# Kernel optimization log

Measured on AMD Instinct MI355X. Metric: run time of the kernel, lower is better.

## Reference

```python
import jax, jax.numpy as jnp
import numpy as np

# static config (matches init_kwargs and spatial_shapes input)
SPATIAL = ((100, 100), (50, 50), (25, 25), (13, 13))  # (H, W) per level
D_MODEL, N_HEADS, N_LEVELS, N_POINTS, D_FFN = 256, 8, 4, 4, 1024
D_HEAD = D_MODEL // N_HEADS
LEN_IN = sum(h * w for h, w in SPATIAL)
LEVEL_START = np.cumsum([0] + [h * w for h, w in SPATIAL])[:-1]


def setup_inputs() -> dict:
    key = jax.random.key(0)
    ks = jax.random.split(key, 12)
    N = 2
    f = lambda k, shape, s=0.02: jax.random.normal(k, shape, jnp.float32) * s
    return {
        "src": jax.random.normal(ks[0], (N, LEN_IN, D_MODEL), jnp.float32),
        "pos": jax.random.normal(ks[1], (N, LEN_IN, D_MODEL), jnp.float32),
        "reference_points": jax.random.uniform(ks[2], (N, LEN_IN, N_LEVELS, 2), jnp.float32),
        "spatial_shapes": jnp.asarray(SPATIAL, jnp.int32),
        "level_start_index": jnp.asarray(LEVEL_START, jnp.int32),
        "W_value": f(ks[3], (D_MODEL, D_MODEL)),
        "b_value": jnp.zeros((D_MODEL,), jnp.float32),
        "W_off": f(ks[4], (D_MODEL, N_HEADS * N_LEVELS * N_POINTS * 2)),
        "b_off": f(ks[5], (N_HEADS * N_LEVELS * N_POINTS * 2,), 0.5),
        "W_attn": f(ks[6], (D_MODEL, N_HEADS * N_LEVELS * N_POINTS)),
        "b_attn": jnp.zeros((N_HEADS * N_LEVELS * N_POINTS,), jnp.float32),
        "W_out": f(ks[7], (D_MODEL, D_MODEL)),
        "b_out": jnp.zeros((D_MODEL,), jnp.float32),
        "W1": f(ks[8], (D_MODEL, D_FFN)),
        "b1": jnp.zeros((D_FFN,), jnp.float32),
        "W2": f(ks[9], (D_FFN, D_MODEL)),
        "b2": jnp.zeros((D_MODEL,), jnp.float32),
        "g1": jnp.ones((D_MODEL,), jnp.float32),
        "be1": jnp.zeros((D_MODEL,), jnp.float32),
        "g2": jnp.ones((D_MODEL,), jnp.float32),
        "be2": jnp.zeros((D_MODEL,), jnp.float32),
    }


def _ln(x, g, b, eps=1e-5):
    mu = x.mean(-1, keepdims=True)
    var = ((x - mu) ** 2).mean(-1, keepdims=True)
    return (x - mu) * jax.lax.rsqrt(var + eps) * g + b


def _bilinear(v, loc, H, W):
    # v: [N, heads, H*W, Dh]; loc: [N, Lq, heads, P, 2] normalized to [0,1]
    # replicates F.grid_sample(align_corners=False, padding_mode='zeros') with grid=2*loc-1
    N, Lq, Hh, P, _ = loc.shape
    x = loc[..., 0] * W - 0.5
    y = loc[..., 1] * H - 0.5
    x0 = jnp.floor(x)
    y0 = jnp.floor(y)
    wx1 = x - x0
    wy1 = y - y0
    x0i = x0.astype(jnp.int32)
    y0i = y0.astype(jnp.int32)
    out = jnp.zeros((N, Lq, Hh, P, v.shape[-1]), v.dtype)
    for dy, dx in ((0, 0), (0, 1), (1, 0), (1, 1)):
        xi = x0i + dx
        yi = y0i + dy
        w = (wx1 if dx else 1.0 - wx1) * (wy1 if dy else 1.0 - wy1)
        valid = (xi >= 0) & (xi < W) & (yi >= 0) & (yi < H)
        idx = jnp.clip(yi, 0, H - 1) * W + jnp.clip(xi, 0, W - 1)  # [N,Lq,Hh,P]
        idx = idx.transpose(0, 2, 1, 3).reshape(N, Hh, Lq * P)
        g = jax.vmap(jax.vmap(lambda vm, im: vm[im]))(v, idx)  # [N,Hh,Lq*P,Dh]
        g = g.reshape(N, Hh, Lq, P, -1).transpose(0, 2, 1, 3, 4)
        out = out + (w * valid)[..., None] * g
    return out


def reference(src, pos, reference_points, spatial_shapes, level_start_index,
              W_value, b_value, W_off, b_off, W_attn, b_attn, W_out, b_out,
              W1, b1, W2, b2, g1, be1, g2, be2):
    N, Lq, _ = src.shape
    value = (src @ W_value + b_value).reshape(N, Lq, N_HEADS, D_HEAD)
    q = src + pos  # with_pos_embed
    off = (q @ W_off + b_off).reshape(N, Lq, N_HEADS, N_LEVELS, N_POINTS, 2)
    attn = (q @ W_attn + b_attn).reshape(N, Lq, N_HEADS, N_LEVELS * N_POINTS)
    attn = jax.nn.softmax(attn, axis=-1).reshape(N, Lq, N_HEADS, N_LEVELS, N_POINTS)
    # offset_normalizer = (W, H) per level
    normalizer = jnp.asarray([[w, h] for h, w in SPATIAL], jnp.float32)
    loc = reference_points[:, :, None, :, None, :] + off / normalizer[None, None, None, :, None, :]
    out = jnp.zeros((N, Lq, N_HEADS, D_HEAD), jnp.float32)
    for l, (H, W) in enumerate(SPATIAL):
        s = int(LEVEL_START[l])
        v_l = value[:, s:s + H * W].transpose(0, 2, 1, 3)  # [N, heads, H*W, Dh]
        samp = _bilinear(v_l, loc[:, :, :, l], H, W)       # [N, Lq, heads, P, Dh]
        out = out + jnp.einsum('nqhp,nqhpc->nqhc', attn[:, :, :, l], samp)
    src2 = out.reshape(N, Lq, D_MODEL) @ W_out + b_out
    x = _ln(src + src2, g1, be1)
    ffn = jax.nn.relu(x @ W1 + b1) @ W2 + b2
    return _ln(x + ffn, g2, be2)
```

## Files before the change

### kernel.cpp

```cpp
#include <hip/hip_runtime.h>
#include <hip/hip_bf16.h>
#include <cstdint>

#define D_MODEL   256
#define N_HEADS   8
#define N_LEVELS  4
#define N_POINTS  4
#define D_FFN     1024
#define D_HEAD    32
#define LEN_IN    13294
#define NBATCH    2
#define M_TOK     (NBATCH * LEN_IN)
#define M_PAD     26624

__constant__ int c_lvl_h[4] = {100, 50, 25, 13};
__constant__ int c_lvl_w[4] = {100, 50, 25, 13};
__constant__ int c_lvl_s[4] = {0, 10000, 12500, 13125};

typedef __attribute__((ext_vector_type(8))) __bf16 bf16x8;
typedef __attribute__((ext_vector_type(4))) __bf16 bf16x4;
typedef __attribute__((ext_vector_type(4))) float  f32x4;
typedef __attribute__((ext_vector_type(4))) uint32_t u32x4;

__device__ __forceinline__ float bflo(uint32_t w) { return __uint_as_float(w << 16); }
__device__ __forceinline__ float bfhi(uint32_t w) { return __uint_as_float(w & 0xffff0000u); }

__device__ __forceinline__ void lds_direct16(const void* g, void* l) {
    __builtin_amdgcn_global_load_lds(
        (const __attribute__((address_space(1))) uint32_t*)(uintptr_t)g,
        (__attribute__((address_space(3))) uint32_t*)(uintptr_t)l,
        16, 0, 0);
}

__global__ __launch_bounds__(256) void prep(
    const float* __restrict__ s0, const float* __restrict__ s1, const float* __restrict__ s2,
    const float* __restrict__ s3, const float* __restrict__ s4, const float* __restrict__ s5,
    __bf16* __restrict__ d0, __bf16* __restrict__ d1, __bf16* __restrict__ d2,
    __bf16* __restrict__ d3, __bf16* __restrict__ d4, __bf16* __restrict__ d5,
    const float* __restrict__ b_off, const float* __restrict__ b_attn,
    float* __restrict__ bias_oa,
    const float4* __restrict__ src, const float4* __restrict__ pos,
    bf16x4* __restrict__ sb, bf16x4* __restrict__ qb, int n4)
{
    const int tid = threadIdx.x;
    const int b = blockIdx.x;
    if (b >= 737) {
        const int i = (b - 737) * 256 + tid;
        if (i >= n4) return;
        const float4 s = src[i];
        const float4 p = pos[i];
        bf16x4 sv = { (__bf16)s.x, (__bf16)s.y, (__bf16)s.z, (__bf16)s.w };
        bf16x4 qv = { (__bf16)(s.x + p.x), (__bf16)(s.y + p.y),
                      (__bf16)(s.z + p.z), (__bf16)(s.w + p.w) };
        sb[i] = sv;
        qb[i] = qv;
        return;
    }
    if (b == 736) {
        if (tid < 256) bias_oa[tid] = b_off[tid];
        if (tid < 128) bias_oa[256 + tid] = b_attn[tid];
        return;
    }
    const int tx = tid & 31;
    const int ty = tid >> 5;
    const int starts[7] = {0, 64, 128, 160, 224, 480, 736};
    const int Ks[6] = {256, 256, 256, 256, 256, 1024};
    const int Ns[6] = {256, 256, 128, 256, 1024, 256};
    const float* srcs[6] = {s0, s1, s2, s3, s4, s5};
    __bf16* dsts[6] = {d0, d1, d2, d3, d4, d5};
    int i = 0;
    while (b >= starts[i + 1]) ++i;
    const int t = b - starts[i];
    const int K = Ks[i], N = Ns[i];
    const float* W = srcs[i];
    __bf16* Wt = dsts[i];
    const int ntx = N >> 5;
    const int n0 = (t % ntx) * 32;
    const int k0 = (t / ntx) * 32;

    __shared__ float tl[32][33];
    #pragma unroll
    for (int j = 0; j < 4; ++j)
        tl[ty + j * 8][tx] = W[(size_t)(k0 + ty + j * 8) * N + n0 + tx];
    __syncthreads();
    #pragma unroll
    for (int j = 0; j < 4; ++j)
        Wt[(size_t)(n0 + ty + j * 8) * K + k0 + tx] = (__bf16)tl[tx][ty + j * 8];
}

template <typename OutT, bool RELU, int NP, int K>
__device__ __forceinline__ void gemm_core(
    const __bf16* __restrict__ A, const __bf16* __restrict__ Bt,
    const float* __restrict__ bias, OutT* __restrict__ C,
    int M, int N, int bm, int bn)
{
    __shared__ __bf16 As[NP * 128 * 32];
    __shared__ __bf16 Bs[NP * 128 * 32];

    const int tid  = threadIdx.x;
    const int lane = tid & 63;
    const int wv   = tid >> 6;
    const int wm   = (wv >> 1) * 64;
    const int wn   = (wv & 1) * 64;
    const int srow = lane >> 2;
    const int skc  = (lane & 3) * 8;
    const int fm   = lane & 15;
    const int fko  = (lane >> 4) * 8;

    f32x4 acc[4][4] = {};

    for (int k0 = 0; k0 < K; k0 += 32 * NP) {
        #pragma unroll
        for (int p = 0; p < NP; ++p) {
            #pragma unroll
            for (int c = 0; c < 2; ++c) {
                const int r = wv * 32 + c * 16;
                lds_direct16(A  + (size_t)(bm + r + srow) * K + k0 + p * 32 + skc, As + p * 4096 + r * 32);
                lds_direct16(Bt + (size_t)(bn + r + srow) * K + k0 + p * 32 + skc, Bs + p * 4096 + r * 32);
            }
        }
        __syncthreads();

        #pragma unroll
        for (int p = 0; p < NP; ++p) {
            bf16x8 af[4], bfr[4];
            #pragma unroll
            for (int t = 0; t < 4; ++t) {
                af[t]  = *(const bf16x8*)(As + p * 4096 + (wm + t * 16 + fm) * 32 + fko);
                bfr[t] = *(const bf16x8*)(Bs + p * 4096 + (wn + t * 16 + fm) * 32 + fko);
            }
            #pragma unroll
            for (int mt = 0; mt < 4; ++mt)
                #pragma unroll
                for (int nt = 0; nt < 4; ++nt)
                    acc[mt][nt] = __builtin_amdgcn_mfma_f32_16x16x32_bf16(
                        af[mt], bfr[nt], acc[mt][nt], 0, 0, 0);
        }
        __syncthreads();
    }

    const int ecol = lane & 15;
    const int erow = (lane >> 4) * 4;
    #pragma unroll
    for (int nt = 0; nt < 4; ++nt) {
        const int col = bn + wn + nt * 16 + ecol;
        const float bv = bias[col];
        #pragma unroll
        for (int mt = 0; mt < 4; ++mt) {
            #pragma unroll
            for (int r = 0; r < 4; ++r) {
                const int row = bm + wm + mt * 16 + erow + r;
                if (row < M) {
                    float v = acc[mt][nt][r] + bv;
                    if (RELU) v = fmaxf(v, 0.f);
                    C[(size_t)row * N + col] = (OutT)v;
                }
            }
        }
    }
}

template <typename OutT, bool RELU, int NP, int K>
__global__ __launch_bounds__(256) void gemm_mfma(
    const __bf16* __restrict__ A, const __bf16* __restrict__ Bt,
    const float* __restrict__ bias, OutT* __restrict__ C, int M, int N)
{
    gemm_core<OutT, RELU, NP, K>(A, Bt, bias, C, M, N, blockIdx.y * 128, blockIdx.x * 128);
}

__global__ __launch_bounds__(256) void gemm_front(
    const __bf16* __restrict__ A0, const __bf16* __restrict__ B0,
    const float* __restrict__ bi0, __bf16* __restrict__ C0,
    const __bf16* __restrict__ A1, const __bf16* __restrict__ B1,
    const float* __restrict__ bi1, __bf16* __restrict__ C1, int M)
{
    const int bx = blockIdx.x;
    if (bx < 2)
        gemm_core<__bf16, false, 2, 256>(A0, B0, bi0, C0, M, 256, blockIdx.y * 128, bx * 128);
    else
        gemm_core<__bf16, false, 2, 256>(A1, B1, bi1, C1, M, 384, blockIdx.y * 128, (bx - 2) * 128);
}

template <typename OutT, int K>
__global__ __launch_bounds__(256) void gemm_ln(
    const __bf16* __restrict__ A, const __bf16* __restrict__ Bt,
    const float* __restrict__ bias, const __bf16* __restrict__ res,
    const float* __restrict__ gamma, const float* __restrict__ beta,
    OutT* __restrict__ Cout, int M)
{
    constexpr int NP = 2;
    __shared__ __bf16 As[NP * 64 * 32];
    __shared__ __bf16 Bs[NP * 256 * 32];
    __shared__ float lnsum[64][4];
    __shared__ float lnsq[64][4];
    __shared__ float lnstat[64][2];

    const int tid  = threadIdx.x;
    const int lane = tid & 63;
    const int wv   = tid >> 6;
    const int bm   = blockIdx.x * 64;
    const int wn   = wv * 64;
    const int srow = lane >> 2;
    const int skc  = (lane & 3) * 8;
    const int fm   = lane & 15;
    const int fko  = (lane >> 4) * 8;

    f32x4 acc[4][4] = {};

    for (int k0 = 0; k0 < K; k0 += 32 * NP) {
        #pragma unroll
        for (int p = 0; p < NP; ++p) {
            if (wv == 0) {  }
            lds_direct16(A + (size_t)(bm + wv * 16 + srow) * K + k0 + p * 32 + skc,
                         As + p * 2048 + (wv * 16) * 32);
            #pragma unroll
            for (int c = 0; c < 4; ++c) {
                const int r = wv * 64 + c * 16;
                lds_direct16(Bt + (size_t)(r + srow) * K + k0 + p * 32 + skc,
                             Bs + p * 8192 + r * 32);
            }
        }
        __syncthreads();

        #pragma unroll
        for (int p = 0; p < NP; ++p) {
            bf16x8 af[4], bfr[4];
            #pragma unroll
            for (int t = 0; t < 4; ++t) {
                af[t]  = *(const bf16x8*)(As + p * 2048 + (t * 16 + fm) * 32 + fko);
                bfr[t] = *(const bf16x8*)(Bs + p * 8192 + (wn + t * 16 + fm) * 32 + fko);
            }
            #pragma unroll
            for (int mt = 0; mt < 4; ++mt)
                #pragma unroll
                for (int nt = 0; nt < 4; ++nt)
                    acc[mt][nt] = __builtin_amdgcn_mfma_f32_16x16x32_bf16(
                        af[mt], bfr[nt], acc[mt][nt], 0, 0, 0);
        }
        __syncthreads();
    }

    const int ecol = lane & 15;
    const int erow = (lane >> 4) * 4;

    float g4[4], b4[4];
    #pragma unroll
    for (int nt = 0; nt < 4; ++nt) {
        const int col = wn + nt * 16 + ecol;
        g4[nt] = gamma[col];
        b4[nt] = beta[col];
        const float bv = bias[col];
        #pragma unroll
        for (int mt = 0; mt < 4; ++mt) {
            #pragma unroll
            for (int r = 0; r < 4; ++r) {
                const int row = bm + mt * 16 + erow + r;
                acc[mt][nt][r] += bv + (float)res[(size_t)row * 256 + col];
            }
        }
    }

    #pragma unroll
    for (int mt = 0; mt < 4; ++mt) {
        #pragma unroll
        for (int r = 0; r < 4; ++r) {
            float s  = acc[mt][0][r] + acc[mt][1][r] + acc[mt][2][r] + acc[mt][3][r];
            float s2 = acc[mt][0][r] * acc[mt][0][r] + acc[mt][1][r] * acc[mt][1][r]
                     + acc[mt][2][r] * acc[mt][2][r] + acc[mt][3][r] * acc[mt][3][r];
            #pragma unroll
            for (int o = 1; o < 16; o <<= 1) {
                s  += __shfl_xor(s, o);
                s2 += __shfl_xor(s2, o);
            }
            if (ecol == 0) {
                const int rl = mt * 16 + erow + r;
                lnsum[rl][wv] = s;
                lnsq[rl][wv]  = s2;
            }
        }
    }
    __syncthreads();
    if (tid < 64) {
        const float s  = lnsum[tid][0] + lnsum[tid][1] + lnsum[tid][2] + lnsum[tid][3];
        const float s2 = lnsq[tid][0] + lnsq[tid][1] + lnsq[tid][2] + lnsq[tid][3];
        const float mu = s * (1.f / 256.f);
        const float var = s2 * (1.f / 256.f) - mu * mu;
        lnstat[tid][0] = mu;
        lnstat[tid][1] = rsqrtf(var + 1e-5f);
    }
    __syncthreads();

    #pragma unroll
    for (int mt = 0; mt < 4; ++mt) {
        #pragma unroll
        for (int r = 0; r < 4; ++r) {
            const int rl = mt * 16 + erow + r;
            const int row = bm + rl;
            const float mu = lnstat[rl][0];
            const float rs = lnstat[rl][1];
            if (row < M) {
                #pragma unroll
                for (int nt = 0; nt < 4; ++nt) {
                    const int col = wn + nt * 16 + ecol;
                    const float o = (acc[mt][nt][r] - mu) * rs * g4[nt] + b4[nt];
                    Cout[(size_t)row * 256 + col] = (OutT)o;
                }
            }
        }
    }
}

__global__ __launch_bounds__(256) void msda_sample(
    const __bf16* __restrict__ value,
    const __bf16* __restrict__ oa,
    const float* __restrict__ refp,
    __bf16* __restrict__ out)
{
    __shared__ uint32_t sc[8][16][8];
    __shared__ float sw[8][16];

    const int row = blockIdx.x;
    const int tid = threadIdx.x;

    uint32_t cidx[4];
    float    cwt[4];
    const int h  = tid >> 4;
    const int lp = tid & 15;

    if (tid < 128) {
        const int l  = lp >> 2;
        const int Ww = c_lvl_w[l];
        const int Hh = c_lvl_h[l];
        const uint32_t opk = *(const uint32_t*)(oa + (size_t)row * 384 + h * 32 + lp * 2);
        const float ox = bflo(opk), oy = bfhi(opk);
        const float rx = refp[((size_t)row * 4 + l) * 2 + 0];
        const float ry = refp[((size_t)row * 4 + l) * 2 + 1];
        const float x = (rx + ox / (float)Ww) * (float)Ww - 0.5f;
        const float y = (ry + oy / (float)Hh) * (float)Hh - 0.5f;
        const float xf = floorf(x), yf = floorf(y);
        const float fx = x - xf,    fy = y - yf;
        const int x0 = (int)xf, y0 = (int)yf;
        const int n  = row / LEN_IN;
        const int base = n * LEN_IN + c_lvl_s[l];
        #pragma unroll
        for (int c = 0; c < 4; ++c) {
            const int dx = c & 1, dy = c >> 1;
            const int xi = x0 + dx, yi = y0 + dy;
            const bool valid = (xi >= 0) & (xi < Ww) & (yi >= 0) & (yi < Hh);
            cidx[c] = valid ? (uint32_t)(base + yi * Ww + xi) * 512u : 0u;
            cwt[c]  = valid ? (dx ? fx : 1.f - fx) * (dy ? fy : 1.f - fy) : 0.f;
        }
    } else if (tid < 136) {
        const int h2 = tid - 128;
        const __bf16* ap = oa + (size_t)row * 384 + 256 + h2 * 16;
        float e[16], mx = -1e30f;
        #pragma unroll
        for (int i = 0; i < 16; ++i) { e[i] = (float)ap[i]; mx = fmaxf(mx, e[i]); }
        float s = 0.f;
        #pragma unroll
        for (int i = 0; i < 16; ++i) { e[i] = __expf(e[i] - mx); s += e[i]; }
        const float inv = 1.f / s;
        #pragma unroll
        for (int i = 0; i < 16; ++i) sw[h2][i] = e[i] * inv;
    }
    __syncthreads();
    if (tid < 128) {
        const float a = sw[h][lp];
        u32x4 pk0 = { cidx[0], __float_as_uint(cwt[0] * a), cidx[1], __float_as_uint(cwt[1] * a) };
        u32x4 pk1 = { cidx[2], __float_as_uint(cwt[2] * a), cidx[3], __float_as_uint(cwt[3] * a) };
        *(u32x4*)&sc[h][lp][0] = pk0;
        *(u32x4*)&sc[h][lp][4] = pk1;
    }
    __syncthreads();

    const char* __restrict__ vb = (const char*)value;
    const int gh  = tid >> 5;
    const uint32_t colb = (uint32_t)tid * 2u;
    float acc = 0.f;
    #pragma unroll
    for (int q = 0; q < 16; ++q) {
        const u32x4 a = *(const u32x4*)&sc[gh][q][0];
        const u32x4 b = *(const u32x4*)&sc[gh][q][4];
        acc += __uint_as_float(a.y) * __uint_as_float((uint32_t)(*(const uint16_t*)(vb + (size_t)(a.x + colb))) << 16);
        acc += __uint_as_float(a.w) * __uint_as_float((uint32_t)(*(const uint16_t*)(vb + (size_t)(a.z + colb))) << 16);
        acc += __uint_as_float(b.y) * __uint_as_float((uint32_t)(*(const uint16_t*)(vb + (size_t)(b.x + colb))) << 16);
        acc += __uint_as_float(b.w) * __uint_as_float((uint32_t)(*(const uint16_t*)(vb + (size_t)(b.z + colb))) << 16);
    }
    out[(size_t)row * 256 + tid] = (__bf16)acc;
}

extern "C" void kernel_launch(void* const* d_in, const int* in_sizes, int n_in,
                              void* d_out, int out_size, void* d_ws, size_t ws_size,
                              hipStream_t stream)
{
    const float* src     = (const float*)d_in[0];
    const float* pos     = (const float*)d_in[1];
    const float* refp    = (const float*)d_in[2];
    const float* W_value = (const float*)d_in[5];
    const float* b_value = (const float*)d_in[6];
    const float* W_off   = (const float*)d_in[7];
    const float* b_off   = (const float*)d_in[8];
    const float* W_attn  = (const float*)d_in[9];
    const float* b_attn  = (const float*)d_in[10];
    const float* W_out   = (const float*)d_in[11];
    const float* b_out   = (const float*)d_in[12];
    const float* W1      = (const float*)d_in[13];
    const float* b1      = (const float*)d_in[14];
    const float* W2      = (const float*)d_in[15];
    const float* b2      = (const float*)d_in[16];
    const float* g1      = (const float*)d_in[17];
    const float* be1     = (const float*)d_in[18];
    const float* g2      = (const float*)d_in[19];
    const float* be2     = (const float*)d_in[20];
    float* outp = (float*)d_out;

    const int M = M_TOK;
    char* ws = (char*)d_ws;
    const size_t R2 = (size_t)M_PAD * 512;

    __bf16* src_b = (__bf16*)(ws);
    __bf16* q_b   = (__bf16*)(ws + R2);
    __bf16* val_b = (__bf16*)(ws + 2 * R2);
    __bf16* oa    = (__bf16*)(ws + 3 * R2);
    __bf16* samp  = (__bf16*)(ws + 9 * R2 / 2);
    __bf16* x_b   = (__bf16*)(ws + 11 * R2 / 2);
    __bf16* hbuf  = (__bf16*)(ws);
    __bf16* wbase = (__bf16*)(ws + 13 * R2 / 2);
    __bf16* Wt_value = wbase;
    __bf16* Wt_oa    = wbase + 65536;
    __bf16* Wt_out   = wbase + 163840;
    __bf16* Wt1      = wbase + 229376;
    __bf16* Wt2      = wbase + 491520;
    float*  bias_oa  = (float*)(wbase + 753664);

    const dim3 blk(256);
    const int n4 = M * 256 / 4;
    const int gm = M_PAD / 128;
    const int gl = M_PAD / 64;

    prep<<<dim3(737 + (n4 + 255) / 256), blk, 0, stream>>>(
        W_value, W_off, W_attn, W_out, W1, W2,
        Wt_value, Wt_oa, Wt_oa + 65536, Wt_out, Wt1, Wt2,
        b_off, b_attn, bias_oa,
        (const float4*)src, (const float4*)pos, (bf16x4*)src_b, (bf16x4*)q_b, n4);

    gemm_front<<<dim3(5, gm), blk, 0, stream>>>(
        src_b, Wt_value, b_value, val_b,
        q_b,   Wt_oa,    bias_oa, oa, M);

    msda_sample<<<dim3(M), blk, 0, stream>>>(val_b, oa, refp, samp);

    gemm_ln<__bf16, 256><<<dim3(gl), blk, 0, stream>>>(
        samp, Wt_out, b_out, src_b, g1, be1, x_b, M);

    gemm_mfma<__bf16, true, 2, 256><<<dim3(8, gm), blk, 0, stream>>>(x_b, Wt1, b1, hbuf, M, 1024);

    gemm_ln<float, 1024><<<dim3(gl), blk, 0, stream>>>(
        hbuf, Wt2, b2, x_b, g2, be2, outp, M);
}
```

Before: 348.2 us.

## Replace LDS-staged GEMM tiles with direct register loads and per-wave tiles

All GEMM kernels drop the LDS staging (global_load_lds plus barriers) and have each wave load its MFMA fragments straight from global memory into registers, with a two-stage register double buffer across K panels. The front and FFN1 GEMMs now assign an independent 64x64 tile to each wave instead of a 128x128 block tile shared by four waves. This removes the LDS traffic and the __syncthreads stalls, but waves no longer share loaded operands, so global/L2 traffic per FLOP goes up and the per-lane 16-byte row loads are strided by K.

Result: slower. 423.2 us (+21.5%).

```diff
diff --git a/kernel.cpp b/kernel.cpp
--- a/kernel.cpp
+++ b/kernel.cpp
@@ -24,13 +24,6 @@
 
 __device__ __forceinline__ float bflo(uint32_t w) { return __uint_as_float(w << 16); }
 __device__ __forceinline__ float bfhi(uint32_t w) { return __uint_as_float(w & 0xffff0000u); }
-
-__device__ __forceinline__ void lds_direct16(const void* g, void* l) {
-    __builtin_amdgcn_global_load_lds(
-        (const __attribute__((address_space(1))) uint32_t*)(uintptr_t)g,
-        (__attribute__((address_space(3))) uint32_t*)(uintptr_t)l,
-        16, 0, 0);
-}
 
 __global__ __launch_bounds__(256) void prep(
     const float* __restrict__ s0, const float* __restrict__ s1, const float* __restrict__ s2,
@@ -88,68 +81,57 @@
         Wt[(size_t)(n0 + ty + j * 8) * K + k0 + tx] = (__bf16)tl[tx][ty + j * 8];
 }
 
-template <typename OutT, bool RELU, int NP, int K>
-__device__ __forceinline__ void gemm_core(
+template <bool RELU, int K, typename OutT>
+__device__ __forceinline__ void gemm_rd_tile(
     const __bf16* __restrict__ A, const __bf16* __restrict__ Bt,
     const float* __restrict__ bias, OutT* __restrict__ C,
-    int M, int N, int bm, int bn)
-{
-    __shared__ __bf16 As[NP * 128 * 32];
-    __shared__ __bf16 Bs[NP * 128 * 32];
-
-    const int tid  = threadIdx.x;
-    const int lane = tid & 63;
-    const int wv   = tid >> 6;
-    const int wm   = (wv >> 1) * 64;
-    const int wn   = (wv & 1) * 64;
-    const int srow = lane >> 2;
-    const int skc  = (lane & 3) * 8;
-    const int fm   = lane & 15;
-    const int fko  = (lane >> 4) * 8;
+    int M, int N, int tm, int tn)
+{
+    const int lane = threadIdx.x & 63;
+    const int fm  = lane & 15;
+    const int fko = (lane >> 4) * 8;
+    const __bf16* Ap = A  + (size_t)(tm * 64 + fm) * K + fko;
+    const __bf16* Bp = Bt + (size_t)(tn * 64 + fm) * K + fko;
 
     f32x4 acc[4][4] = {};
-
-    for (int k0 = 0; k0 < K; k0 += 32 * NP) {
-        #pragma unroll
-        for (int p = 0; p < NP; ++p) {
-            #pragma unroll
-            for (int c = 0; c < 2; ++c) {
-                const int r = wv * 32 + c * 16;
-                lds_direct16(A  + (size_t)(bm + r + srow) * K + k0 + p * 32 + skc, As + p * 4096 + r * 32);
-                lds_direct16(Bt + (size_t)(bn + r + srow) * K + k0 + p * 32 + skc, Bs + p * 4096 + r * 32);
-            }
-        }
-        __syncthreads();
-
-        #pragma unroll
-        for (int p = 0; p < NP; ++p) {
-            bf16x8 af[4], bfr[4];
+    bf16x8 af[2][4], bfv[2][4];
+    #pragma unroll
+    for (int t = 0; t < 4; ++t) {
+        af[0][t]  = *(const bf16x8*)(Ap + (size_t)(t * 16) * K);
+        bfv[0][t] = *(const bf16x8*)(Bp + (size_t)(t * 16) * K);
+    }
+    constexpr int NPAN = K / 32;
+    #pragma unroll
+    for (int p = 0; p < NPAN; ++p) {
+        const int cur = p & 1;
+        const int nxt = cur ^ 1;
+        if (p + 1 < NPAN) {
+            const int ko = (p + 1) * 32;
             #pragma unroll
             for (int t = 0; t < 4; ++t) {
-                af[t]  = *(const bf16x8*)(As + p * 4096 + (wm + t * 16 + fm) * 32 + fko);
-                bfr[t] = *(const bf16x8*)(Bs + p * 4096 + (wn + t * 16 + fm) * 32 + fko);
-            }
-            #pragma unroll
-            for (int mt = 0; mt < 4; ++mt)
-                #pragma unroll
-                for (int nt = 0; nt < 4; ++nt)
-                    acc[mt][nt] = __builtin_amdgcn_mfma_f32_16x16x32_bf16(
-                        af[mt], bfr[nt], acc[mt][nt], 0, 0, 0);
-        }
-        __syncthreads();
+                af[nxt][t]  = *(const bf16x8*)(Ap + (size_t)(t * 16) * K + ko);
+                bfv[nxt][t] = *(const bf16x8*)(Bp + (size_t)(t * 16) * K + ko);
+            }
+        }
+        #pragma unroll
+        for (int mt = 0; mt < 4; ++mt)
+            #pragma unroll
+            for (int nt = 0; nt < 4; ++nt)
+                acc[mt][nt] = __builtin_amdgcn_mfma_f32_16x16x32_bf16(
+                    af[cur][mt], bfv[cur][nt], acc[mt][nt], 0, 0, 0);
     }
 
     const int ecol = lane & 15;
     const int erow = (lane >> 4) * 4;
     #pragma unroll
     for (int nt = 0; nt < 4; ++nt) {
-        const int col = bn + wn + nt * 16 + ecol;
+        const int col = tn * 64 + nt * 16 + ecol;
         const float bv = bias[col];
         #pragma unroll
         for (int mt = 0; mt < 4; ++mt) {
             #pragma unroll
             for (int r = 0; r < 4; ++r) {
-                const int row = bm + wm + mt * 16 + erow + r;
+                const int row = tm * 64 + mt * 16 + erow + r;
                 if (row < M) {
                     float v = acc[mt][nt][r] + bv;
                     if (RELU) v = fmaxf(v, 0.f);
@@ -160,37 +142,36 @@
     }
 }
 
-template <typename OutT, bool RELU, int NP, int K>
-__global__ __launch_bounds__(256) void gemm_mfma(
-    const __bf16* __restrict__ A, const __bf16* __restrict__ Bt,
-    const float* __restrict__ bias, OutT* __restrict__ C, int M, int N)
-{
-    gemm_core<OutT, RELU, NP, K>(A, Bt, bias, C, M, N, blockIdx.y * 128, blockIdx.x * 128);
-}
-
-__global__ __launch_bounds__(256) void gemm_front(
+__global__ __launch_bounds__(256) void gemm_front_rd(
     const __bf16* __restrict__ A0, const __bf16* __restrict__ B0,
     const float* __restrict__ bi0, __bf16* __restrict__ C0,
     const __bf16* __restrict__ A1, const __bf16* __restrict__ B1,
     const float* __restrict__ bi1, __bf16* __restrict__ C1, int M)
 {
-    const int bx = blockIdx.x;
-    if (bx < 2)
-        gemm_core<__bf16, false, 2, 256>(A0, B0, bi0, C0, M, 256, blockIdx.y * 128, bx * 128);
-    else
-        gemm_core<__bf16, false, 2, 256>(A1, B1, bi1, C1, M, 384, blockIdx.y * 128, (bx - 2) * 128);
+    const int w = blockIdx.x * 4 + (threadIdx.x >> 6);
+    if (w < 1664) {
+        gemm_rd_tile<false, 256, __bf16>(A0, B0, bi0, C0, M, 256, w >> 2, w & 3);
+    } else {
+        const int t = w - 1664;
+        gemm_rd_tile<false, 256, __bf16>(A1, B1, bi1, C1, M, 384, t / 6, t % 6);
+    }
+}
+
+__global__ __launch_bounds__(256) void gemm_ffn1_rd(
+    const __bf16* __restrict__ A, const __bf16* __restrict__ Bt,
+    const float* __restrict__ bias, __bf16* __restrict__ C, int M)
+{
+    const int w = blockIdx.x * 4 + (threadIdx.x >> 6);
+    gemm_rd_tile<true, 256, __bf16>(A, Bt, bias, C, M, 1024, w >> 4, w & 15);
 }
 
 template <typename OutT, int K>
-__global__ __launch_bounds__(256) void gemm_ln(
+__global__ __launch_bounds__(256) void gemm_ln_rd(
     const __bf16* __restrict__ A, const __bf16* __restrict__ Bt,
     const float* __restrict__ bias, const __bf16* __restrict__ res,
     const float* __restrict__ gamma, const float* __restrict__ beta,
     OutT* __restrict__ Cout, int M)
 {
-    constexpr int NP = 2;
-    __shared__ __bf16 As[NP * 64 * 32];
-    __shared__ __bf16 Bs[NP * 256 * 32];
     __shared__ float lnsum[64][4];
     __shared__ float lnsq[64][4];
     __shared__ float lnstat[64][2];
@@ -200,44 +181,37 @@
     const int wv   = tid >> 6;
     const int bm   = blockIdx.x * 64;
     const int wn   = wv * 64;
-    const int srow = lane >> 2;
-    const int skc  = (lane & 3) * 8;
     const int fm   = lane & 15;
     const int fko  = (lane >> 4) * 8;
+    const __bf16* Ap = A  + (size_t)(bm + fm) * K + fko;
+    const __bf16* Bp = Bt + (size_t)(wn + fm) * K + fko;
 
     f32x4 acc[4][4] = {};
-
-    for (int k0 = 0; k0 < K; k0 += 32 * NP) {
-        #pragma unroll
-        for (int p = 0; p < NP; ++p) {
-            if (wv == 0) {  }
-            lds_direct16(A + (size_t)(bm + wv * 16 + srow) * K + k0 + p * 32 + skc,
-                         As + p * 2048 + (wv * 16) * 32);
-            #pragma unroll
-            for (int c = 0; c < 4; ++c) {
-                const int r = wv * 64 + c * 16;
-                lds_direct16(Bt + (size_t)(r + srow) * K + k0 + p * 32 + skc,
-                             Bs + p * 8192 + r * 32);
-            }
-        }
-        __syncthreads();
-
-        #pragma unroll
-        for (int p = 0; p < NP; ++p) {
-            bf16x8 af[4], bfr[4];
+    bf16x8 af[2][4], bfv[2][4];
+    #pragma unroll
+    for (int t = 0; t < 4; ++t) {
+        af[0][t]  = *(const bf16x8*)(Ap + (size_t)(t * 16) * K);
+        bfv[0][t] = *(const bf16x8*)(Bp + (size_t)(t * 16) * K);
+    }
+    constexpr int NPAN = K / 32;
+    #pragma unroll
+    for (int p = 0; p < NPAN; ++p) {
+        const int cur = p & 1;
+        const int nxt = cur ^ 1;
+        if (p + 1 < NPAN) {
+            const int ko = (p + 1) * 32;
             #pragma unroll
             for (int t = 0; t < 4; ++t) {
-                af[t]  = *(const bf16x8*)(As + p * 2048 + (t * 16 + fm) * 32 + fko);
-                bfr[t] = *(const bf16x8*)(Bs + p * 8192 + (wn + t * 16 + fm) * 32 + fko);
-            }
-            #pragma unroll
-            for (int mt = 0; mt < 4; ++mt)
-                #pragma unroll
-                for (int nt = 0; nt < 4; ++nt)
-                    acc[mt][nt] = __builtin_amdgcn_mfma_f32_16x16x32_bf16(
-                        af[mt], bfr[nt], acc[mt][nt], 0, 0, 0);
-        }
-        __syncthreads();
+                af[nxt][t]  = *(const bf16x8*)(Ap + (size_t)(t * 16) * K + ko);
+                bfv[nxt][t] = *(const bf16x8*)(Bp + (size_t)(t * 16) * K + ko);
+            }
+        }
+        #pragma unroll
+        for (int mt = 0; mt < 4; ++mt)
+            #pragma unroll
+            for (int nt = 0; nt < 4; ++nt)
+                acc[mt][nt] = __builtin_amdgcn_mfma_f32_16x16x32_bf16(
+                    af[cur][mt], bfv[cur][nt], acc[mt][nt], 0, 0, 0);
     }
 
     const int ecol = lane & 15;
@@ -435,8 +409,6 @@
 
     const dim3 blk(256);
     const int n4 = M * 256 / 4;
-    const int gm = M_PAD / 128;
-    const int gl = M_PAD / 64;
 
     prep<<<dim3(737 + (n4 + 255) / 256), blk, 0, stream>>>(
         W_value, W_off, W_attn, W_out, W1, W2,
@@ -444,17 +416,17 @@
         b_off, b_attn, bias_oa,
         (const float4*)src, (const float4*)pos, (bf16x4*)src_b, (bf16x4*)q_b, n4);
 
-    gemm_front<<<dim3(5, gm), blk, 0, stream>>>(
+    gemm_front_rd<<<dim3(1040), blk, 0, stream>>>(
         src_b, Wt_value, b_value, val_b,
         q_b,   Wt_oa,    bias_oa, oa, M);
 
     msda_sample<<<dim3(M), blk, 0, stream>>>(val_b, oa, refp, samp);
 
-    gemm_ln<__bf16, 256><<<dim3(gl), blk, 0, stream>>>(
+    gemm_ln_rd<__bf16, 256><<<dim3(M_PAD / 64), blk, 0, stream>>>(
         samp, Wt_out, b_out, src_b, g1, be1, x_b, M);
 
-    gemm_mfma<__bf16, true, 2, 256><<<dim3(8, gm), blk, 0, stream>>>(x_b, Wt1, b1, hbuf, M, 1024);
-
-    gemm_ln<float, 1024><<<dim3(gl), blk, 0, stream>>>(
+    gemm_ffn1_rd<<<dim3(1664), blk, 0, stream>>>(x_b, Wt1, b1, hbuf, M);
+
+    gemm_ln_rd<float, 1024><<<dim3(M_PAD / 64), blk, 0, stream>>>(
         hbuf, Wt2, b2, x_b, g2, be2, outp, M);
 }
```

## Stage GEMM epilogues through LDS for vector stores and halve LN-GEMM row tile

Applied to the files above, without the earlier changes.

GEMM epilogues now write results into shared memory and then emit coalesced 16-byte row stores, instead of scattered scalar stores in the MFMA fragment layout. The fused GEMM+LayerNorm kernels drop from 64-row to 32-row tiles, doubling the block count to improve occupancy and load balance, at the cost of reloading the full B tile twice as often. Shared memory use grows for the padded staging buffers, and each epilogue gains an extra barrier.

Measured after the change: 305.7 us. -12.2%, faster.

```diff
diff --git a/kernel.cpp b/kernel.cpp
--- a/kernel.cpp
+++ b/kernel.cpp
@@ -88,14 +88,15 @@
         Wt[(size_t)(n0 + ty + j * 8) * K + k0 + tx] = (__bf16)tl[tx][ty + j * 8];
 }
 
-template <typename OutT, bool RELU, int NP, int K>
+template <bool RELU, int K>
 __device__ __forceinline__ void gemm_core(
     const __bf16* __restrict__ A, const __bf16* __restrict__ Bt,
-    const float* __restrict__ bias, OutT* __restrict__ C,
+    const float* __restrict__ bias, __bf16* __restrict__ C,
     int M, int N, int bm, int bn)
 {
-    __shared__ __bf16 As[NP * 128 * 32];
-    __shared__ __bf16 Bs[NP * 128 * 32];
+    __shared__ __bf16 smem[17408];
+    __bf16* As = smem;
+    __bf16* Bs = smem + 8192;
 
     const int tid  = threadIdx.x;
     const int lane = tid & 63;
@@ -109,9 +110,9 @@
 
     f32x4 acc[4][4] = {};
 
-    for (int k0 = 0; k0 < K; k0 += 32 * NP) {
-        #pragma unroll
-        for (int p = 0; p < NP; ++p) {
+    for (int k0 = 0; k0 < K; k0 += 64) {
+        #pragma unroll
+        for (int p = 0; p < 2; ++p) {
             #pragma unroll
             for (int c = 0; c < 2; ++c) {
                 const int r = wv * 32 + c * 16;
@@ -122,7 +123,7 @@
         __syncthreads();
 
         #pragma unroll
-        for (int p = 0; p < NP; ++p) {
+        for (int p = 0; p < 2; ++p) {
             bf16x8 af[4], bfr[4];
             #pragma unroll
             for (int t = 0; t < 4; ++t) {
@@ -143,29 +144,29 @@
     const int erow = (lane >> 4) * 4;
     #pragma unroll
     for (int nt = 0; nt < 4; ++nt) {
-        const int col = bn + wn + nt * 16 + ecol;
-        const float bv = bias[col];
+        const int cl = wn + nt * 16 + ecol;
+        const float bv = bias[bn + cl];
         #pragma unroll
         for (int mt = 0; mt < 4; ++mt) {
             #pragma unroll
             for (int r = 0; r < 4; ++r) {
-                const int row = bm + wm + mt * 16 + erow + r;
-                if (row < M) {
-                    float v = acc[mt][nt][r] + bv;
-                    if (RELU) v = fmaxf(v, 0.f);
-                    C[(size_t)row * N + col] = (OutT)v;
-                }
-            }
-        }
-    }
-}
-
-template <typename OutT, bool RELU, int NP, int K>
-__global__ __launch_bounds__(256) void gemm_mfma(
-    const __bf16* __restrict__ A, const __bf16* __restrict__ Bt,
-    const float* __restrict__ bias, OutT* __restrict__ C, int M, int N)
-{
-    gemm_core<OutT, RELU, NP, K>(A, Bt, bias, C, M, N, blockIdx.y * 128, blockIdx.x * 128);
+                const int rl = wm + mt * 16 + erow + r;
+                float v = acc[mt][nt][r] + bv;
+                if (RELU) v = fmaxf(v, 0.f);
+                smem[rl * 136 + cl] = (__bf16)v;
+            }
+        }
+    }
+    __syncthreads();
+    #pragma unroll
+    for (int rr = 0; rr < 8; ++rr) {
+        const int idx = rr * 256 + tid;
+        const int row = idx >> 4;
+        const int ch  = idx & 15;
+        if (bm + row < M)
+            *(bf16x8*)(C + (size_t)(bm + row) * N + bn + ch * 8) =
+                *(const bf16x8*)(smem + row * 136 + ch * 8);
+    }
 }
 
 __global__ __launch_bounds__(256) void gemm_front(
@@ -176,43 +177,53 @@
 {
     const int bx = blockIdx.x;
     if (bx < 2)
-        gemm_core<__bf16, false, 2, 256>(A0, B0, bi0, C0, M, 256, blockIdx.y * 128, bx * 128);
+        gemm_core<false, 256>(A0, B0, bi0, C0, M, 256, blockIdx.y * 128, bx * 128);
     else
-        gemm_core<__bf16, false, 2, 256>(A1, B1, bi1, C1, M, 384, blockIdx.y * 128, (bx - 2) * 128);
+        gemm_core<false, 256>(A1, B1, bi1, C1, M, 384, blockIdx.y * 128, (bx - 2) * 128);
+}
+
+__global__ __launch_bounds__(256) void gemm_ffn1(
+    const __bf16* __restrict__ A, const __bf16* __restrict__ Bt,
+    const float* __restrict__ bias, __bf16* __restrict__ C, int M)
+{
+    gemm_core<true, 256>(A, Bt, bias, C, M, 1024, blockIdx.y * 128, blockIdx.x * 128);
 }
 
 template <typename OutT, int K>
-__global__ __launch_bounds__(256) void gemm_ln(
+__global__ __launch_bounds__(256) void gemm_ln32(
     const __bf16* __restrict__ A, const __bf16* __restrict__ Bt,
     const float* __restrict__ bias, const __bf16* __restrict__ res,
     const float* __restrict__ gamma, const float* __restrict__ beta,
     OutT* __restrict__ Cout, int M)
 {
-    constexpr int NP = 2;
-    __shared__ __bf16 As[NP * 64 * 32];
-    __shared__ __bf16 Bs[NP * 256 * 32];
-    __shared__ float lnsum[64][4];
-    __shared__ float lnsq[64][4];
-    __shared__ float lnstat[64][2];
+    __shared__ __bf16 smem[18432];
+    __bf16* As = smem;
+    __bf16* Bs = smem + 2048;
+    __shared__ float lnsum[32][4];
+    __shared__ float lnsq[32][4];
+    __shared__ float lnstat[32][2];
 
     const int tid  = threadIdx.x;
     const int lane = tid & 63;
     const int wv   = tid >> 6;
-    const int bm   = blockIdx.x * 64;
+    const int bm   = blockIdx.x * 32;
     const int wn   = wv * 64;
     const int srow = lane >> 2;
     const int skc  = (lane & 3) * 8;
     const int fm   = lane & 15;
     const int fko  = (lane >> 4) * 8;
 
-    f32x4 acc[4][4] = {};
-
-    for (int k0 = 0; k0 < K; k0 += 32 * NP) {
-        #pragma unroll
-        for (int p = 0; p < NP; ++p) {
-            if (wv == 0) {  }
-            lds_direct16(A + (size_t)(bm + wv * 16 + srow) * K + k0 + p * 32 + skc,
-                         As + p * 2048 + (wv * 16) * 32);
+    f32x4 acc[2][4] = {};
+
+    for (int k0 = 0; k0 < K; k0 += 64) {
+        {
+            const int p  = wv >> 1;
+            const int rh = (wv & 1) * 16;
+            lds_direct16(A + (size_t)(bm + rh + srow) * K + k0 + p * 32 + skc,
+                         As + p * 1024 + rh * 32);
+        }
+        #pragma unroll
+        for (int p = 0; p < 2; ++p) {
             #pragma unroll
             for (int c = 0; c < 4; ++c) {
                 const int r = wv * 64 + c * 16;
@@ -223,15 +234,16 @@
         __syncthreads();
 
         #pragma unroll
-        for (int p = 0; p < NP; ++p) {
-            bf16x8 af[4], bfr[4];
-            #pragma unroll
-            for (int t = 0; t < 4; ++t) {
-                af[t]  = *(const bf16x8*)(As + p * 2048 + (t * 16 + fm) * 32 + fko);
-                bfr[t] = *(const bf16x8*)(Bs + p * 8192 + (wn + t * 16 + fm) * 32 + fko);
-            }
-            #pragma unroll
-            for (int mt = 0; mt < 4; ++mt)
+        for (int p = 0; p < 2; ++p) {
+            bf16x8 af[2], bfr[4];
+            #pragma unroll
+            for (int mt = 0; mt < 2; ++mt)
+                af[mt] = *(const bf16x8*)(As + p * 1024 + (mt * 16 + fm) * 32 + fko);
+            #pragma unroll
+            for (int nt = 0; nt < 4; ++nt)
+                bfr[nt] = *(const bf16x8*)(Bs + p * 8192 + (wn + nt * 16 + fm) * 32 + fko);
+            #pragma unroll
+            for (int mt = 0; mt < 2; ++mt)
                 #pragma unroll
                 for (int nt = 0; nt < 4; ++nt)
                     acc[mt][nt] = __builtin_amdgcn_mfma_f32_16x16x32_bf16(
@@ -251,7 +263,7 @@
         b4[nt] = beta[col];
         const float bv = bias[col];
         #pragma unroll
-        for (int mt = 0; mt < 4; ++mt) {
+        for (int mt = 0; mt < 2; ++mt) {
             #pragma unroll
             for (int r = 0; r < 4; ++r) {
                 const int row = bm + mt * 16 + erow + r;
@@ -261,7 +273,7 @@
     }
 
     #pragma unroll
-    for (int mt = 0; mt < 4; ++mt) {
+    for (int mt = 0; mt < 2; ++mt) {
         #pragma unroll
         for (int r = 0; r < 4; ++r) {
             float s  = acc[mt][0][r] + acc[mt][1][r] + acc[mt][2][r] + acc[mt][3][r];
@@ -280,7 +292,7 @@
         }
     }
     __syncthreads();
-    if (tid < 64) {
+    if (tid < 32) {
         const float s  = lnsum[tid][0] + lnsum[tid][1] + lnsum[tid][2] + lnsum[tid][3];
         const float s2 = lnsq[tid][0] + lnsq[tid][1] + lnsq[tid][2] + lnsq[tid][3];
         const float mu = s * (1.f / 256.f);
@@ -290,21 +302,57 @@
     }
     __syncthreads();
 
-    #pragma unroll
-    for (int mt = 0; mt < 4; ++mt) {
-        #pragma unroll
-        for (int r = 0; r < 4; ++r) {
-            const int rl = mt * 16 + erow + r;
-            const int row = bm + rl;
-            const float mu = lnstat[rl][0];
-            const float rs = lnstat[rl][1];
-            if (row < M) {
+    if constexpr (sizeof(OutT) == 2) {
+        __bf16* ct = smem;
+        #pragma unroll
+        for (int mt = 0; mt < 2; ++mt) {
+            #pragma unroll
+            for (int r = 0; r < 4; ++r) {
+                const int rl = mt * 16 + erow + r;
+                const float mu = lnstat[rl][0];
+                const float rs = lnstat[rl][1];
                 #pragma unroll
                 for (int nt = 0; nt < 4; ++nt) {
                     const int col = wn + nt * 16 + ecol;
-                    const float o = (acc[mt][nt][r] - mu) * rs * g4[nt] + b4[nt];
-                    Cout[(size_t)row * 256 + col] = (OutT)o;
+                    ct[rl * 264 + col] = (__bf16)((acc[mt][nt][r] - mu) * rs * g4[nt] + b4[nt]);
                 }
+            }
+        }
+        __syncthreads();
+        #pragma unroll
+        for (int rr = 0; rr < 4; ++rr) {
+            const int idx = rr * 256 + tid;
+            const int row = idx >> 5;
+            const int ch  = idx & 31;
+            if (bm + row < M)
+                *(bf16x8*)((__bf16*)Cout + (size_t)(bm + row) * 256 + ch * 8) =
+                    *(const bf16x8*)(ct + row * 264 + ch * 8);
+        }
+    } else {
+        float* ct = (float*)smem;
+        #pragma unroll
+        for (int mt = 0; mt < 2; ++mt) {
+            #pragma unroll
+            for (int r = 0; r < 4; ++r) {
+                const int rl = mt * 16 + erow + r;
+                const float mu = lnstat[rl][0];
+                const float rs = lnstat[rl][1];
+                #pragma unroll
+                for (int nt = 0; nt < 4; ++nt) {
+                    const int col = wn + nt * 16 + ecol;
+                    ct[rl * 260 + col] = (acc[mt][nt][r] - mu) * rs * g4[nt] + b4[nt];
+                }
+            }
+        }
+        __syncthreads();
+        #pragma unroll
+        for (int rr = 0; rr < 8; ++rr) {
+            const int idx = rr * 256 + tid;
+            const int row = idx >> 6;
+            const int ch  = idx & 63;
+            if (bm + row < M) {
+                float4 v = *(const float4*)(ct + row * 260 + ch * 4);
+                *(float4*)((float*)Cout + (size_t)(bm + row) * 256 + ch * 4) = v;
             }
         }
     }
@@ -436,7 +484,6 @@
     const dim3 blk(256);
     const int n4 = M * 256 / 4;
     const int gm = M_PAD / 128;
-    const int gl = M_PAD / 64;
 
     prep<<<dim3(737 + (n4 + 255) / 256), blk, 0, stream>>>(
         W_value, W_off, W_attn, W_out, W1, W2,
@@ -450,11 +497,11 @@
 
     msda_sample<<<dim3(M), blk, 0, stream>>>(val_b, oa, refp, samp);
 
-    gemm_ln<__bf16, 256><<<dim3(gl), blk, 0, stream>>>(
+    gemm_ln32<__bf16, 256><<<dim3(M_PAD / 32), blk, 0, stream>>>(
         samp, Wt_out, b_out, src_b, g1, be1, x_b, M);
 
-    gemm_mfma<__bf16, true, 2, 256><<<dim3(8, gm), blk, 0, stream>>>(x_b, Wt1, b1, hbuf, M, 1024);
-
-    gemm_ln<float, 1024><<<dim3(gl), blk, 0, stream>>>(
+    gemm_ffn1<<<dim3(8, gm), blk, 0, stream>>>(x_b, Wt1, b1, hbuf, M);
+
+    gemm_ln32<float, 1024><<<dim3(M_PAD / 32), blk, 0, stream>>>(
         hbuf, Wt2, b2, x_b, g2, be2, outp, M);
 }
```
